# Kernel tuning notes

Hardware: AMD Instinct MI355X
Metric: run time of the kernel (lower is better)

The kernel has to match this reference:

```python
import jax, jax.numpy as jnp
import numpy as np

D_MODEL = 1024
N_HEADS = 16
D_K = D_MODEL // N_HEADS
ROPE_BASE = 500000.0
RMS_EPS = 1e-10


def _rms_norm(x, w):
    # RMSNorm over last dim (per-head d_k): w * x / sqrt(mean(x^2) + eps)
    rms = jnp.sqrt(jnp.mean(x * x, axis=-1, keepdims=True) + RMS_EPS)
    return w * (x / rms)


def _rotate_half(x):
    x1, x2 = x[..., : x.shape[-1] // 2], x[..., x.shape[-1] // 2:]
    return jnp.concatenate([-x2, x1], axis=-1)


def _rope_cos_sin(seq_len):
    inv_freq = 1.0 / (ROPE_BASE ** (jnp.arange(0, D_K, 2, dtype=jnp.float32) / D_K))
    t = jnp.arange(seq_len, dtype=jnp.float32)
    freqs = jnp.outer(t, inv_freq)                # (S, d_k/2)
    emb = jnp.concatenate([freqs, freqs], axis=-1)  # (S, d_k)
    return jnp.cos(emb), jnp.sin(emb)


def setup_inputs() -> dict:
    key = jax.random.key(0)
    ks = jax.random.split(key, 9)
    B, S, D = 2, 2048, D_MODEL
    scale = 1.0 / np.sqrt(D)
    return {
        "q": jax.random.normal(ks[0], (B, S, D), jnp.float32),
        "k": jax.random.normal(ks[1], (B, S, D), jnp.float32),
        "v": jax.random.normal(ks[2], (B, S, D), jnp.float32),
        "w_q": jax.random.normal(ks[3], (D, D), jnp.float32) * scale,
        "w_k": jax.random.normal(ks[4], (D, D), jnp.float32) * scale,
        "w_v": jax.random.normal(ks[5], (D, D), jnp.float32) * scale,
        "w_o": jax.random.normal(ks[6], (D, D), jnp.float32) * scale,
        "q_norm_w": jnp.ones((D_K,), jnp.float32),
        "k_norm_w": jnp.ones((D_K,), jnp.float32),
    }


def reference(q, k, v, w_q, w_k, w_v, w_o, q_norm_w, k_norm_w):
    B, S, D = q.shape
    H, Dk = N_HEADS, D_K

    # QKV projections (nn.Linear without bias: x @ W.T), split into heads
    query = jnp.einsum("bsd,ed->bse", q, w_q).reshape(B, S, H, Dk).transpose(0, 2, 1, 3)
    key_ = jnp.einsum("bsd,ed->bse", k, w_k).reshape(B, S, H, Dk).transpose(0, 2, 1, 3)
    value = jnp.einsum("bsd,ed->bse", v, w_v).reshape(B, S, H, Dk).transpose(0, 2, 1, 3)

    # QK-norm (per-head RMSNorm)
    query = _rms_norm(query, q_norm_w)
    key_ = _rms_norm(key_, k_norm_w)

    # RoPE, default positions 0..S-1
    cos, sin = _rope_cos_sin(S)          # (S, d_k)
    cos = cos[None, None]                # (1,1,S,d_k)
    sin = sin[None, None]
    query = query * cos + _rotate_half(query) * sin
    key_ = key_ * cos + _rotate_half(key_) * sin

    # Causal scaled dot-product attention
    scale = 1.0 / jnp.sqrt(jnp.asarray(Dk, query.dtype))
    scores = jnp.einsum("bhqd,bhkd->bhqk", query, key_) * scale
    causal = jnp.tril(jnp.ones((S, S), dtype=bool))
    scores = jnp.where(causal, scores, jnp.finfo(scores.dtype).min)
    attn = jax.nn.softmax(scores, axis=-1)
    out = jnp.einsum("bhqk,bhkd->bhqd", attn, value)  # (B,H,S,d_k)

    out = out.transpose(0, 2, 1, 3).reshape(B, S, D)
    return jnp.einsum("bsd,ed->bse", out, w_o)
```

## Files before the change

kernel.cpp:

```cpp
#include <hip/hip_runtime.h>
#include <cstdint>
#include <cstddef>

typedef __bf16 bf16;
typedef __bf16 bf16x4_t __attribute__((ext_vector_type(4)));
typedef __bf16 bf16x8_t __attribute__((ext_vector_type(8)));
typedef float  f32x4_t  __attribute__((ext_vector_type(4)));

#define GLD_LDS16(g, l)                                                              \
  __builtin_amdgcn_global_load_lds((const __attribute__((address_space(1))) void*)(g), \
                                   (__attribute__((address_space(3))) void*)(l), 16, 0, 0)

#define S_WAITCNT_VMCNT(N) asm volatile("s_waitcnt vmcnt(" #N ")" ::: "memory")
#define S_BARRIER() asm volatile("s_barrier" ::: "memory")

__global__ __launch_bounds__(256) void cvt_kernel(
    const float* __restrict__ q, const float* __restrict__ k, const float* __restrict__ v,
    const float* __restrict__ wq, const float* __restrict__ wk, const float* __restrict__ wv,
    const float* __restrict__ wo,
    bf16* __restrict__ qb, bf16* __restrict__ kb, bf16* __restrict__ vb,
    bf16* __restrict__ wqb, bf16* __restrict__ wkb, bf16* __restrict__ wvb,
    bf16* __restrict__ wob)
{
  const float* src; bf16* dst; int n;
  switch (blockIdx.y) {
    case 0: src = q;  dst = qb;  n = 4194304; break;
    case 1: src = k;  dst = kb;  n = 4194304; break;
    case 2: src = v;  dst = vb;  n = 4194304; break;
    case 3: src = wq; dst = wqb; n = 1048576; break;
    case 4: src = wk; dst = wkb; n = 1048576; break;
    case 5: src = wv; dst = wvb; n = 1048576; break;
    default: src = wo; dst = wob; n = 1048576; break;
  }
  const int i = (blockIdx.x * 256 + threadIdx.x) * 4;
  if (i >= n) return;
  const float4 f = *(const float4*)(src + i);
  bf16x4_t o;
  o[0] = (bf16)f.x; o[1] = (bf16)f.y; o[2] = (bf16)f.z; o[3] = (bf16)f.w;
  *(bf16x4_t*)(dst + i) = o;
}

template <typename OUT_T>
__device__ __forceinline__ void gemm_body(const bf16* __restrict__ A,
                                          const bf16* __restrict__ W,
                                          OUT_T* __restrict__ C)
{
  const int K = 1024, N = 1024;
  __shared__ bf16 As[3][128 * 32];
  __shared__ bf16 Bs[3][128 * 32];
  const int t = threadIdx.x;
  const int lane = t & 63, w = t >> 6;
  const int l16 = lane & 15, qd = lane >> 4;
  const int m0 = blockIdx.y * 128, n0 = blockIdx.x * 128;
  const int wm = (w & 1) * 64, wn = (w >> 1) * 64;

  f32x4_t acc[4][4] = {};

  const int srow = t >> 2;
  const int scol = ((t & 3) ^ (srow & 3)) * 8;
  const bf16* ag0 = A + (size_t)(m0 + srow) * K + scol;
  const bf16* ag1 = A + (size_t)(m0 + 64 + srow) * K + scol;
  const bf16* wg0 = W + (size_t)(n0 + srow) * K + scol;
  const bf16* wg1 = W + (size_t)(n0 + 64 + srow) * K + scol;
  const int lo0 = (w * 64) * 8;
  const int lo1 = (256 + w * 64) * 8;

  const int sw = l16 & 3;

#define STAGEG(k0_, b_)                         \
  do {                                          \
    GLD_LDS16(ag0 + (k0_), &As[b_][lo0]);       \
    GLD_LDS16(ag1 + (k0_), &As[b_][lo1]);       \
    GLD_LDS16(wg0 + (k0_), &Bs[b_][lo0]);       \
    GLD_LDS16(wg1 + (k0_), &Bs[b_][lo1]);       \
  } while (0)

  STAGEG(0, 0);
  STAGEG(32, 1);

  for (int k0 = 0; k0 < K; k0 += 32) {
    const int it = k0 >> 5;
    const int cb = it - (it / 3) * 3;
    if (k0 + 32 < K) S_WAITCNT_VMCNT(4); else S_WAITCNT_VMCNT(0);
    S_BARRIER();
    if (k0 + 64 < K) {
      const int nb = (it + 2) - ((it + 2) / 3) * 3;
      STAGEG(k0 + 64, nb);
    }
    bf16x8_t af[4], bfg[4];
#pragma unroll
    for (int i = 0; i < 4; ++i)
      af[i] = *(const bf16x8_t*)(&As[cb][(wm + i * 16 + l16) * 32 + (qd ^ sw) * 8]);
#pragma unroll
    for (int j = 0; j < 4; ++j)
      bfg[j] = *(const bf16x8_t*)(&Bs[cb][(wn + j * 16 + l16) * 32 + (qd ^ sw) * 8]);
#pragma unroll
    for (int i = 0; i < 4; ++i)
#pragma unroll
      for (int j = 0; j < 4; ++j)
        acc[i][j] = __builtin_amdgcn_mfma_f32_16x16x32_bf16(af[i], bfg[j], acc[i][j], 0, 0, 0);
  }
#undef STAGEG

#pragma unroll
  for (int i = 0; i < 4; ++i) {
    const int row = m0 + wm + i * 16 + qd * 4;
#pragma unroll
    for (int j = 0; j < 4; ++j) {
      const int col = n0 + wn + j * 16 + l16;
#pragma unroll
      for (int r = 0; r < 4; ++r)
        C[(size_t)(row + r) * N + col] = (OUT_T)acc[i][j][r];
    }
  }
}

__global__ __launch_bounds__(256) void gemm_proj(
    const bf16* qb, const bf16* wqb, bf16* Yq,
    const bf16* kb, const bf16* wkb, bf16* Yk,
    const bf16* vb, const bf16* wvb, bf16* Yv)
{
  const bf16 *A, *W; bf16* C;
  if (blockIdx.z == 0)      { A = qb; W = wqb; C = Yq; }
  else if (blockIdx.z == 1) { A = kb; W = wkb; C = Yk; }
  else                      { A = vb; W = wvb; C = Yv; }
  gemm_body<bf16>(A, W, C);
}

__global__ __launch_bounds__(256) void gemm_out_k(
    const bf16* __restrict__ Ob, const bf16* __restrict__ wob, float* __restrict__ out)
{
  gemm_body<float>(Ob, wob, out);
}

__global__ __launch_bounds__(256) void prep_kernel(
    const bf16* __restrict__ Yq, const bf16* __restrict__ Yk, const bf16* __restrict__ Yv,
    const float* __restrict__ qnw, const float* __restrict__ knw,
    bf16* __restrict__ Qp, bf16* __restrict__ Kp, bf16* __restrict__ Vt)
{
  if (blockIdx.y == 2) {
    if (blockIdx.x >= 1024) return;
    __shared__ bf16 T[64][80];
    const int st = blockIdx.x & 31;
    const int bh = blockIdx.x >> 5;
    const int b = bh >> 4, h = bh & 15;
    const int t = threadIdx.x;
#pragma unroll
    for (int p = 0; p < 2; ++p) {
      const int r = p * 32 + (t >> 3);
      const int c8 = (t & 7) * 8;
      const bf16x8_t v =
          *(const bf16x8_t*)(Yv + ((size_t)(b * 2048 + st * 64 + r)) * 1024 + h * 64 + c8);
#pragma unroll
      for (int j = 0; j < 8; ++j) T[c8 + j][r] = v[j];
    }
    __syncthreads();
#pragma unroll
    for (int p = 0; p < 2; ++p) {
      const int c = p * 32 + (t >> 3);
      const int r8 = (t & 7) * 8;
      const bf16x8_t v = *(const bf16x8_t*)(&T[c][r8]);
      const int base32 = st * 64 + (r8 & 32);
      const int k0 = r8 & 31;
      const int p0 = 8 * ((k0 & 15) >> 2) + ((k0 >= 16) ? 4 : 0);
      const int k1 = k0 + 4;
      const int p1 = 8 * ((k1 & 15) >> 2) + ((k1 >= 16) ? 4 : 0);
      bf16* dst = Vt + ((size_t)(bh * 64 + c)) * 2048;
      bf16x4_t lo, hi;
#pragma unroll
      for (int j = 0; j < 4; ++j) { lo[j] = v[j]; hi[j] = v[4 + j]; }
      *(bf16x4_t*)(dst + base32 + p0) = lo;
      *(bf16x4_t*)(dst + base32 + p1) = hi;
    }
    return;
  }

  const bf16* Y; const float* nw; bf16* Out; float oscale;
  if (blockIdx.y == 0) { Y = Yq; nw = qnw; Out = Qp; oscale = 0.125f * 1.44269504088896f; }
  else                 { Y = Yk; nw = knw; Out = Kp; oscale = 1.0f; }

  const int row = blockIdx.x * 4 + (threadIdx.x >> 6);
  const int lane = threadIdx.x & 63;
  const int h = row & 15;
  const int bs = row >> 4;
  const int s = bs & 2047;
  const int b = bs >> 11;

  float x = (float)Y[(size_t)row * 64 + lane];
  float ss = x * x;
#pragma unroll
  for (int off = 32; off > 0; off >>= 1) ss += __shfl_xor(ss, off);
  const float rms = sqrtf(ss * (1.0f / 64.0f) + 1e-10f);
  const float xn = (x / rms) * nw[lane];
  const float other = __shfl_xor(xn, 32);
  const int i = lane & 31;
  const float invf_rev =
      __builtin_amdgcn_exp2f(-(float)(2 * i) * (18.93156857f / 64.0f)) * 0.15915494309f;
  float rev = (float)s * invf_rev;
  rev = rev - floorf(rev);
  const float cv = __builtin_amdgcn_cosf(rev);
  const float sv = __builtin_amdgcn_sinf(rev);
  const float rot = (lane < 32) ? -other : other;
  const float val = (xn * cv + rot * sv) * oscale;
  Out[((size_t)(b * 16 + h) * 2048 + s) * 64 + lane] = (bf16)val;
}

__global__ __launch_bounds__(512) void flash_attn(
    const bf16* __restrict__ Qp, const bf16* __restrict__ Kp,
    const bf16* __restrict__ Vt, bf16* __restrict__ O)
{
  const int S = 2048;
  const int qt = 15 - blockIdx.x;
  const int bh = blockIdx.y;
  const int t = threadIdx.x;
  const int lane = t & 63, w = t >> 6;
  const int l16 = lane & 15, qd = lane >> 4;

  __shared__ bf16 Ks[3][64 * 64];
  __shared__ bf16 Vs[3][64 * 64];

  const int qrow = qt * 128 + w * 16 + l16;
  const bf16* qbase = Qp + ((size_t)bh * S + qrow) * 64 + qd * 8;
  const bf16x8_t qf0 = *(const bf16x8_t*)qbase;
  const bf16x8_t qf1 = *(const bf16x8_t*)(qbase + 32);

  f32x4_t o_acc[4] = {};
  float l_i = 0.f;

  const int srow = t >> 3;
  const int scol = ((t & 7) ^ (srow & 7)) * 8;
  const bf16* kg = Kp + ((size_t)bh * S + srow) * 64 + scol;
  const bf16* vg = Vt + ((size_t)(bh * 64 + srow)) * S + scol;
  const int lo = w * 512;

  const int sw = l16 & 7;

#define STAGE(kt_, b_)                                 \
  do {                                                 \
    GLD_LDS16(kg + (size_t)(kt_) * 4096, &Ks[b_][lo]); \
    GLD_LDS16(vg + (kt_) * 64, &Vs[b_][lo]);           \
  } while (0)

  const int ktmax = 2 * qt + 1;
  STAGE(0, 0);
  STAGE(1, 1);

  for (int kt = 0; kt <= ktmax; ++kt) {
    const int cb = kt - (kt / 3) * 3;
    if (kt < ktmax) S_WAITCNT_VMCNT(2); else S_WAITCNT_VMCNT(0);
    S_BARRIER();
    if (kt + 2 <= ktmax) {
      const int nb = (kt + 2) - ((kt + 2) / 3) * 3;
      STAGE(kt + 2, nb);
    }

    if (kt == ktmax && w < 4) continue;

    f32x4_t sf[4];
#pragma unroll
    for (int nt = 0; nt < 4; ++nt) {
      sf[nt][0] = -12.f; sf[nt][1] = -12.f; sf[nt][2] = -12.f; sf[nt][3] = -12.f;
      const bf16x8_t kf0 = *(const bf16x8_t*)(&Ks[cb][(nt * 16 + l16) * 64 + ((0 + qd) ^ sw) * 8]);
      const bf16x8_t kf1 = *(const bf16x8_t*)(&Ks[cb][(nt * 16 + l16) * 64 + ((4 + qd) ^ sw) * 8]);
      sf[nt] = __builtin_amdgcn_mfma_f32_16x16x32_bf16(kf0, qf0, sf[nt], 0, 0, 0);
      sf[nt] = __builtin_amdgcn_mfma_f32_16x16x32_bf16(kf1, qf1, sf[nt], 0, 0, 0);
    }

    if (kt >= ktmax - 1) {
      const int kofs = (kt - 2 * qt) * 64;
      const int q_local = w * 16 + l16;
#pragma unroll
      for (int nt = 0; nt < 4; ++nt)
#pragma unroll
        for (int r = 0; r < 4; ++r)
          if (kofs + nt * 16 + qd * 4 + r > q_local) sf[nt][r] = -100.f;
    }

    bf16x4_t pb[4];
#pragma unroll
    for (int nt = 0; nt < 4; ++nt)
#pragma unroll
      for (int r = 0; r < 4; ++r) {
        const float p = __builtin_amdgcn_exp2f(sf[nt][r]);
        l_i += p;
        pb[nt][r] = (bf16)p;
      }

#pragma unroll
    for (int nt2 = 0; nt2 < 2; ++nt2) {
      bf16x8_t pf;
#pragma unroll
      for (int r = 0; r < 4; ++r) { pf[r] = pb[2 * nt2][r]; pf[4 + r] = pb[2 * nt2 + 1][r]; }
#pragma unroll
      for (int dt = 0; dt < 4; ++dt) {
        const int row = dt * 16 + l16;
        const bf16x8_t vf =
            *(const bf16x8_t*)(&Vs[cb][row * 64 + ((4 * nt2 + qd) ^ sw) * 8]);
        o_acc[dt] = __builtin_amdgcn_mfma_f32_16x16x32_bf16(vf, pf, o_acc[dt], 0, 0, 0);
      }
    }
  }
#undef STAGE

  l_i += __shfl_xor(l_i, 16);
  l_i += __shfl_xor(l_i, 32);

  const int b = bh >> 4, h = bh & 15;
  const float inv_l = 1.0f / l_i;
  const int qg = qt * 128 + w * 16 + l16;
#pragma unroll
  for (int dt = 0; dt < 4; ++dt) {
    bf16x4_t ov;
#pragma unroll
    for (int r = 0; r < 4; ++r) ov[r] = (bf16)(o_acc[dt][r] * inv_l);
    *(bf16x4_t*)(O + ((size_t)(b * S + qg)) * 1024 + h * 64 + dt * 16 + qd * 4) = ov;
  }
}

extern "C" void kernel_launch(void* const* d_in, const int* in_sizes, int n_in,
                              void* d_out, int out_size, void* d_ws, size_t ws_size,
                              hipStream_t stream)
{
  const float* q   = (const float*)d_in[0];
  const float* k   = (const float*)d_in[1];
  const float* v   = (const float*)d_in[2];
  const float* wq  = (const float*)d_in[3];
  const float* wk  = (const float*)d_in[4];
  const float* wv  = (const float*)d_in[5];
  const float* wo  = (const float*)d_in[6];
  const float* qnw = (const float*)d_in[7];
  const float* knw = (const float*)d_in[8];

  char* ws = (char*)d_ws;
  const size_t MB = 1u << 20;
  bf16* qb  = (bf16*)(ws + 0 * MB);
  bf16* kb  = (bf16*)(ws + 8 * MB);
  bf16* vb  = (bf16*)(ws + 16 * MB);
  bf16* wqb = (bf16*)(ws + 24 * MB);
  bf16* wkb = (bf16*)(ws + 26 * MB);
  bf16* wvb = (bf16*)(ws + 28 * MB);
  bf16* wob = (bf16*)(ws + 30 * MB);
  bf16* Yq  = (bf16*)(ws + 32 * MB);
  bf16* Yk  = (bf16*)(ws + 40 * MB);
  bf16* Yv  = (bf16*)(ws + 48 * MB);
  bf16* Qp    = qb;
  bf16* Kp    = kb;
  bf16* Vtr   = vb;
  bf16* Oattn = Yq;

  cvt_kernel<<<dim3(4096, 7), 256, 0, stream>>>(q, k, v, wq, wk, wv, wo,
                                                qb, kb, vb, wqb, wkb, wvb, wob);
  gemm_proj<<<dim3(8, 32, 3), 256, 0, stream>>>(qb, wqb, Yq, kb, wkb, Yk, vb, wvb, Yv);
  prep_kernel<<<dim3(16384, 3), 256, 0, stream>>>(Yq, Yk, Yv, qnw, knw, Qp, Kp, Vtr);
  flash_attn<<<dim3(16, 32), 512, 0, stream>>>(Qp, Kp, Vtr, Oattn);
  gemm_out_k<<<dim3(8, 32), 256, 0, stream>>>(Oattn, wob, (float*)d_out);
}
```

Baseline: 237.6 us.

## Fuse QK RMSNorm, RoPE and V transpose into QKV projection GEMM epilogue

Removes the separate prep kernel by applying per-head RMSNorm, RoPE and Q scaling directly on the GEMM accumulators. Each warp's 64-column tile maps to one head, and row sums come from lane shuffles. V is written straight into the permuted transposed layout that attention expects. This also changes the LDS swizzle to a two-level XOR key to cut bank conflicts. It saves one full write and read of the projected Q/K/V intermediates and a kernel launch, at the cost of scattered 2-byte stores in the Q/K epilogue and more register pressure.

```diff
diff --git a/kernel.cpp b/kernel.cpp
--- a/kernel.cpp
+++ b/kernel.cpp
@@ -40,24 +40,21 @@
   *(bf16x4_t*)(dst + i) = o;
 }
 
-template <typename OUT_T>
-__device__ __forceinline__ void gemm_body(const bf16* __restrict__ A,
+__device__ __forceinline__ void gemm_core(const bf16* __restrict__ A,
                                           const bf16* __restrict__ W,
-                                          OUT_T* __restrict__ C)
-{
-  const int K = 1024, N = 1024;
+                                          int m0, int n0, f32x4_t (&acc)[4][4])
+{
+  const int K = 1024;
   __shared__ bf16 As[3][128 * 32];
   __shared__ bf16 Bs[3][128 * 32];
   const int t = threadIdx.x;
   const int lane = t & 63, w = t >> 6;
   const int l16 = lane & 15, qd = lane >> 4;
-  const int m0 = blockIdx.y * 128, n0 = blockIdx.x * 128;
   const int wm = (w & 1) * 64, wn = (w >> 1) * 64;
 
-  f32x4_t acc[4][4] = {};
-
   const int srow = t >> 2;
-  const int scol = ((t & 3) ^ (srow & 3)) * 8;
+  const int skey = (srow & 3) ^ ((srow >> 2) & 3);
+  const int scol = ((t & 3) ^ skey) * 8;
   const bf16* ag0 = A + (size_t)(m0 + srow) * K + scol;
   const bf16* ag1 = A + (size_t)(m0 + 64 + srow) * K + scol;
   const bf16* wg0 = W + (size_t)(n0 + srow) * K + scol;
@@ -65,7 +62,7 @@
   const int lo0 = (w * 64) * 8;
   const int lo1 = (256 + w * 64) * 8;
 
-  const int sw = l16 & 3;
+  const int sw = (l16 & 3) ^ ((l16 >> 2) & 3);
 
 #define STAGEG(k0_, b_)                         \
   do {                                          \
@@ -101,7 +98,117 @@
         acc[i][j] = __builtin_amdgcn_mfma_f32_16x16x32_bf16(af[i], bfg[j], acc[i][j], 0, 0, 0);
   }
 #undef STAGEG
-
+}
+
+__global__ __launch_bounds__(256) void gemm_qkv(
+    const bf16* __restrict__ qb, const bf16* __restrict__ wqb,
+    const bf16* __restrict__ kb, const bf16* __restrict__ wkb,
+    const bf16* __restrict__ vb, const bf16* __restrict__ wvb,
+    const float* __restrict__ qnw, const float* __restrict__ knw,
+    bf16* __restrict__ Qp, bf16* __restrict__ Kp, bf16* __restrict__ Vt)
+{
+  const int z = blockIdx.z;
+  const bf16 *A, *W;
+  if (z == 0)      { A = qb; W = wqb; }
+  else if (z == 1) { A = kb; W = wkb; }
+  else             { A = vb; W = wvb; }
+
+  const int m0 = blockIdx.y * 128, n0 = blockIdx.x * 128;
+  f32x4_t acc[4][4] = {};
+  gemm_core(A, W, m0, n0, acc);
+
+  const int t = threadIdx.x;
+  const int lane = t & 63, w = t >> 6;
+  const int l16 = lane & 15, qd = lane >> 4;
+  const int wm = (w & 1) * 64;
+  const int h = blockIdx.x * 2 + (w >> 1);
+  const int b = m0 >> 11;
+
+  if (z == 2) {
+#pragma unroll
+    for (int i = 0; i < 4; ++i) {
+      const int sq = (m0 & 2047) + wm + i * 16 + qd * 4;
+      const int pos = (sq & ~31) + 8 * qd + 4 * (i & 1);
+#pragma unroll
+      for (int j = 0; j < 4; ++j) {
+        const int dk = j * 16 + l16;
+        bf16x4_t ov;
+#pragma unroll
+        for (int r = 0; r < 4; ++r) ov[r] = (bf16)acc[i][j][r];
+        *(bf16x4_t*)(Vt + ((size_t)((b * 16 + h) * 64 + dk)) * 2048 + pos) = ov;
+      }
+    }
+    return;
+  }
+
+  const float* nw = (z == 0) ? qnw : knw;
+  const float osc = (z == 0) ? 0.125f * 1.44269504088896f : 1.0f;
+  bf16* Out = (z == 0) ? Qp : Kp;
+
+  float nwv[4];
+#pragma unroll
+  for (int j = 0; j < 4; ++j) nwv[j] = nw[j * 16 + l16];
+  float invf[2];
+#pragma unroll
+  for (int jj = 0; jj < 2; ++jj) {
+    const int d = jj * 16 + l16;
+    invf[jj] = __builtin_amdgcn_exp2f(-(float)(2 * d) * (18.93156857f / 64.0f)) * 0.15915494309f;
+  }
+
+#pragma unroll
+  for (int i = 0; i < 4; ++i) {
+    const int sbase = (m0 & 2047) + wm + i * 16 + qd * 4;
+    float ssq[4];
+#pragma unroll
+    for (int r = 0; r < 4; ++r) {
+      ssq[r] = 0.f;
+#pragma unroll
+      for (int j = 0; j < 4; ++j) ssq[r] += acc[i][j][r] * acc[i][j][r];
+    }
+#pragma unroll
+    for (int off = 1; off < 16; off <<= 1)
+#pragma unroll
+      for (int r = 0; r < 4; ++r) ssq[r] += __shfl_xor(ssq[r], off);
+
+    float xn[4][4];
+#pragma unroll
+    for (int r = 0; r < 4; ++r) {
+      const float inv = 1.0f / sqrtf(ssq[r] * (1.0f / 64.0f) + 1e-10f);
+#pragma unroll
+      for (int j = 0; j < 4; ++j) xn[j][r] = acc[i][j][r] * inv * nwv[j];
+    }
+#pragma unroll
+    for (int jj = 0; jj < 2; ++jj) {
+      const int d = jj * 16 + l16;
+#pragma unroll
+      for (int r = 0; r < 4; ++r) {
+        const int s = sbase + r;
+        float rev = (float)s * invf[jj];
+        rev = rev - floorf(rev);
+        const float cv = __builtin_amdgcn_cosf(rev);
+        const float sv = __builtin_amdgcn_sinf(rev);
+        const float o1 = (xn[jj][r] * cv - xn[jj + 2][r] * sv) * osc;
+        const float o2 = (xn[jj + 2][r] * cv + xn[jj][r] * sv) * osc;
+        bf16* base = Out + ((size_t)(b * 16 + h) * 2048 + s) * 64;
+        base[d] = (bf16)o1;
+        base[d + 32] = (bf16)o2;
+      }
+    }
+  }
+}
+
+__global__ __launch_bounds__(256) void gemm_out_k(
+    const bf16* __restrict__ Ob, const bf16* __restrict__ wob, float* __restrict__ out)
+{
+  const int N = 1024;
+  const int m0 = blockIdx.y * 128, n0 = blockIdx.x * 128;
+  f32x4_t acc[4][4] = {};
+  gemm_core(Ob, wob, m0, n0, acc);
+
+  const int t = threadIdx.x;
+  const int lane = t & 63, w = t >> 6;
+  const int l16 = lane & 15, qd = lane >> 4;
+  const int wm = (w & 1) * 64, wn = (w >> 1) * 64;
 #pragma unroll
   for (int i = 0; i < 4; ++i) {
     const int row = m0 + wm + i * 16 + qd * 4;
@@ -110,99 +217,9 @@
       const int col = n0 + wn + j * 16 + l16;
 #pragma unroll
       for (int r = 0; r < 4; ++r)
-        C[(size_t)(row + r) * N + col] = (OUT_T)acc[i][j][r];
-    }
-  }
-}
-
-__global__ __launch_bounds__(256) void gemm_proj(
-    const bf16* qb, const bf16* wqb, bf16* Yq,
-    const bf16* kb, const bf16* wkb, bf16* Yk,
-    const bf16* vb, const bf16* wvb, bf16* Yv)
-{
-  const bf16 *A, *W; bf16* C;
-  if (blockIdx.z == 0)      { A = qb; W = wqb; C = Yq; }
-  else if (blockIdx.z == 1) { A = kb; W = wkb; C = Yk; }
-  else                      { A = vb; W = wvb; C = Yv; }
-  gemm_body<bf16>(A, W, C);
-}
-
-__global__ __launch_bounds__(256) void gemm_out_k(
-    const bf16* __restrict__ Ob, const bf16* __restrict__ wob, float* __restrict__ out)
-{
-  gemm_body<float>(Ob, wob, out);
-}
-
-__global__ __launch_bounds__(256) void prep_kernel(
-    const bf16* __restrict__ Yq, const bf16* __restrict__ Yk, const bf16* __restrict__ Yv,
-    const float* __restrict__ qnw, const float* __restrict__ knw,
-    bf16* __restrict__ Qp, bf16* __restrict__ Kp, bf16* __restrict__ Vt)
-{
-  if (blockIdx.y == 2) {
-    if (blockIdx.x >= 1024) return;
-    __shared__ bf16 T[64][80];
-    const int st = blockIdx.x & 31;
-    const int bh = blockIdx.x >> 5;
-    const int b = bh >> 4, h = bh & 15;
-    const int t = threadIdx.x;
-#pragma unroll
-    for (int p = 0; p < 2; ++p) {
-      const int r = p * 32 + (t >> 3);
-      const int c8 = (t & 7) * 8;
-      const bf16x8_t v =
-          *(const bf16x8_t*)(Yv + ((size_t)(b * 2048 + st * 64 + r)) * 1024 + h * 64 + c8);
-#pragma unroll
-      for (int j = 0; j < 8; ++j) T[c8 + j][r] = v[j];
-    }
-    __syncthreads();
-#pragma unroll
-    for (int p = 0; p < 2; ++p) {
-      const int c = p * 32 + (t >> 3);
-      const int r8 = (t & 7) * 8;
-      const bf16x8_t v = *(const bf16x8_t*)(&T[c][r8]);
-      const int base32 = st * 64 + (r8 & 32);
-      const int k0 = r8 & 31;
-      const int p0 = 8 * ((k0 & 15) >> 2) + ((k0 >= 16) ? 4 : 0);
-      const int k1 = k0 + 4;
-      const int p1 = 8 * ((k1 & 15) >> 2) + ((k1 >= 16) ? 4 : 0);
-      bf16* dst = Vt + ((size_t)(bh * 64 + c)) * 2048;
-      bf16x4_t lo, hi;
-#pragma unroll
-      for (int j = 0; j < 4; ++j) { lo[j] = v[j]; hi[j] = v[4 + j]; }
-      *(bf16x4_t*)(dst + base32 + p0) = lo;
-      *(bf16x4_t*)(dst + base32 + p1) = hi;
-    }
-    return;
-  }
-
-  const bf16* Y; const float* nw; bf16* Out; float oscale;
-  if (blockIdx.y == 0) { Y = Yq; nw = qnw; Out = Qp; oscale = 0.125f * 1.44269504088896f; }
-  else                 { Y = Yk; nw = knw; Out = Kp; oscale = 1.0f; }
-
-  const int row = blockIdx.x * 4 + (threadIdx.x >> 6);
-  const int lane = threadIdx.x & 63;
-  const int h = row & 15;
-  const int bs = row >> 4;
-  const int s = bs & 2047;
-  const int b = bs >> 11;
-
-  float x = (float)Y[(size_t)row * 64 + lane];
-  float ss = x * x;
-#pragma unroll
-  for (int off = 32; off > 0; off >>= 1) ss += __shfl_xor(ss, off);
-  const float rms = sqrtf(ss * (1.0f / 64.0f) + 1e-10f);
-  const float xn = (x / rms) * nw[lane];
-  const float other = __shfl_xor(xn, 32);
-  const int i = lane & 31;
-  const float invf_rev =
-      __builtin_amdgcn_exp2f(-(float)(2 * i) * (18.93156857f / 64.0f)) * 0.15915494309f;
-  float rev = (float)s * invf_rev;
-  rev = rev - floorf(rev);
-  const float cv = __builtin_amdgcn_cosf(rev);
-  const float sv = __builtin_amdgcn_sinf(rev);
-  const float rot = (lane < 32) ? -other : other;
-  const float val = (xn * cv + rot * sv) * oscale;
-  Out[((size_t)(b * 16 + h) * 2048 + s) * 64 + lane] = (bf16)val;
+        out[(size_t)(row + r) * N + col] = acc[i][j][r];
+    }
+  }
 }
 
 __global__ __launch_bounds__(512) void flash_attn(
@@ -340,18 +357,15 @@
   bf16* wkb = (bf16*)(ws + 26 * MB);
   bf16* wvb = (bf16*)(ws + 28 * MB);
   bf16* wob = (bf16*)(ws + 30 * MB);
-  bf16* Yq  = (bf16*)(ws + 32 * MB);
-  bf16* Yk  = (bf16*)(ws + 40 * MB);
-  bf16* Yv  = (bf16*)(ws + 48 * MB);
-  bf16* Qp    = qb;
-  bf16* Kp    = kb;
-  bf16* Vtr   = vb;
-  bf16* Oattn = Yq;
+  bf16* Qp  = (bf16*)(ws + 32 * MB);
+  bf16* Kp  = (bf16*)(ws + 40 * MB);
+  bf16* Vtr = (bf16*)(ws + 48 * MB);
+  bf16* Oattn = qb;
 
   cvt_kernel<<<dim3(4096, 7), 256, 0, stream>>>(q, k, v, wq, wk, wv, wo,
                                                 qb, kb, vb, wqb, wkb, wvb, wob);
-  gemm_proj<<<dim3(8, 32, 3), 256, 0, stream>>>(qb, wqb, Yq, kb, wkb, Yk, vb, wvb, Yv);
-  prep_kernel<<<dim3(16384, 3), 256, 0, stream>>>(Yq, Yk, Yv, qnw, knw, Qp, Kp, Vtr);
+  gemm_qkv<<<dim3(8, 32, 3), 256, 0, stream>>>(qb, wqb, kb, wkb, vb, wvb,
+                                               qnw, knw, Qp, Kp, Vtr);
   flash_attn<<<dim3(16, 32), 512, 0, stream>>>(Qp, Kp, Vtr, Oattn);
   gemm_out_k<<<dim3(8, 32), 256, 0, stream>>>(Oattn, wob, (float*)d_out);
 }
```

After: 226.9 us. 1.05x faster.
